# Optimization experiments

Measured on AMD Instinct MI355X. Metric: run time of the kernel, lower is better.

Reference implementation:

```python
import jax, jax.numpy as jnp
import numpy as np

INPUT_DIM = 2048
EMBED_DIM = 128


def setup_inputs() -> dict:
    key = jax.random.key(0)
    kx, kw, kb, kv = jax.random.split(key, 4)
    x = jax.random.normal(kx, (16384, INPUT_DIM), dtype=jnp.float32)
    # nn.Linear(input_dim, 1): weight [1, D] (init std=0.01), bias [1]
    W = jax.random.normal(kw, (1, INPUT_DIM), dtype=jnp.float32) * 0.01
    b = jax.random.normal(kb, (1,), dtype=jnp.float32) * 0.01
    # nn.Embedding(input_dim, embedding_dim): V [D, K] (init std=0.01)
    V = jax.random.normal(kv, (INPUT_DIM, EMBED_DIM), dtype=jnp.float32) * 0.01
    return {"x": x, "W": W, "b": b, "V": V}


def reference(x, W, b, V):
    # linear part: x @ W^T + b -> [B, 1]
    linear_part = x @ W.T + b
    # FM 2nd-order interaction via the standard identity:
    # 0.5 * sum_k ( (sum_d x_d V_dk)^2 - sum_d x_d^2 V_dk^2 )
    # equals the original sum_square - square_sum over weighted embeddings.
    xv = x @ V                       # [B, K]
    x2v2 = (x * x) @ (V * V)         # [B, K]
    interaction = 0.5 * jnp.sum(xv * xv - x2v2, axis=1, keepdims=True)
    return linear_part + interaction
```

## Files before the change

### kernel.cpp

```cpp
#include <hip/hip_runtime.h>
#include <hip/hip_bf16.h>

#define K_DIM 2048
#define N_DIM 128
#define BM 32
#define BK 64
#define NTILES (K_DIM / BK)
#define VT_CHUNK 16384

typedef __bf16 bf16x8 __attribute__((ext_vector_type(8)));
typedef float f32x4 __attribute__((ext_vector_type(4)));

__device__ __forceinline__ float dot4(f32x4 a, f32x4 b) {
    return a.x * b.x + a.y * b.y + a.z * b.z + a.w * b.w;
}

__device__ __forceinline__ void gload16(const void* g, void* lds) {
    __builtin_amdgcn_global_load_lds(
        (const __attribute__((address_space(1))) unsigned int*)g,
        (__attribute__((address_space(3))) unsigned int*)lds,
        16, 0, 0);
}

__global__ __launch_bounds__(256) void fm_prep(const float* __restrict__ V,
                                               char* __restrict__ VtS,
                                               float* __restrict__ s) {
    __shared__ float tile[64][132];
    const int t = threadIdx.x;
    const int kb = blockIdx.x;
    const int k0 = kb * 64;
#pragma unroll
    for (int i = 0; i < 8; ++i) {
        int idx = i * 256 + t;
        int kk = idx >> 5;
        int nq = (idx & 31) * 4;
        *(f32x4*)&tile[kk][nq] = *(const f32x4*)(V + (size_t)(k0 + kk) * N_DIM + nq);
    }
    __syncthreads();
    {
        const int n = t >> 1;
        const int half = t & 1;
        const int sw = (n & 7) << 4;
        char* dstbase = VtS + (size_t)kb * VT_CHUNK + n * 128;
#pragma unroll
        for (int g = 0; g < 4; ++g) {
            int kkg = half * 32 + g * 8;
            bf16x8 o;
#pragma unroll
            for (int e = 0; e < 8; ++e) o[e] = (__bf16)tile[kkg + e][n];
            *(bf16x8*)(dstbase + ((kkg * 2) ^ sw)) = o;
        }
    }
    if (t < 64) {
        float a = 0.f;
#pragma unroll
        for (int nq = 0; nq < 32; ++nq) {
            f32x4 v = *(f32x4*)&tile[t][nq * 4];
            a += dot4(v, v);
        }
        s[k0 + t] = a;
    }
}

__global__ __launch_bounds__(512, 4) void fm_main(const float* __restrict__ x,
                                                  const float* __restrict__ W,
                                                  const float* __restrict__ bptr,
                                                  const char* __restrict__ VtS,
                                                  const float* __restrict__ s,
                                                  float* __restrict__ out) {
    __shared__ __align__(16) char xbuf[2][8192];
    __shared__ __align__(16) char vbuf[2][16384];
    __shared__ __align__(16) float Wl[2048];
    __shared__ __align__(16) float Sl[2048];
    __shared__ float lin_lds[2][16];
    __shared__ float sq_lds[2][16];
    __shared__ float ss_lds[2][4][16];

    const int tid = threadIdx.x;
    const int w = tid >> 6;
    const int l = tid & 63;
    const int lr = l & 15;
    const int lg = l >> 4;
    const int wr = w >> 2;
    const int wc = w & 3;
    const int row0 = blockIdx.x * BM;

    *(f32x4*)&Wl[tid * 4] = *(const f32x4*)(W + tid * 4);
    *(f32x4*)&Sl[tid * 4] = *(const f32x4*)(s + tid * 4);

    const bool isX = (w < 4);
    const char* src[4];
    int loff[4];
    if (isX) {
#pragma unroll
        for (int j = 0; j < 2; ++j) {
            int gi = w * 2 + j;
            int rowt = gi * 4 + lg;
            int koff = (lr * 16) ^ ((rowt & 7) << 4);
            src[j] = (const char*)x + (size_t)(row0 + rowt) * (K_DIM * 4) + koff;
            loff[j] = gi * 1024;
        }
    } else {
#pragma unroll
        for (int j = 0; j < 4; ++j) {
            int vi = (w - 4) * 4 + j;
            src[j] = VtS + vi * 1024 + l * 16;
            loff[j] = vi * 1024;
        }
    }

    f32x4 acc[2];
    acc[0] = (f32x4){0.f, 0.f, 0.f, 0.f};
    acc[1] = (f32x4){0.f, 0.f, 0.f, 0.f};
    float lin = 0.f, sq = 0.f;

    if (isX) {
#pragma unroll
        for (int j = 0; j < 2; ++j) gload16(src[j], &xbuf[0][loff[j]]);
    } else {
#pragma unroll
        for (int j = 0; j < 4; ++j) gload16(src[j], &vbuf[0][loff[j]]);
    }
    __syncthreads();

    const int rowt = wr * 16 + lr;
    const int swA = (rowt & 7) << 4;

    for (int t = 0; t < NTILES; ++t) {
        const int cur = t & 1;
        if (t < NTILES - 1) {
            if (isX) {
#pragma unroll
                for (int j = 0; j < 2; ++j)
                    gload16(src[j] + (size_t)(t + 1) * (BK * 4), &xbuf[cur ^ 1][loff[j]]);
            } else {
#pragma unroll
                for (int j = 0; j < 4; ++j)
                    gload16(src[j] + (size_t)(t + 1) * VT_CHUNK, &vbuf[cur ^ 1][loff[j]]);
            }
        }

        const char* arow = &xbuf[cur][0] + rowt * 256;
        const char* vb = &vbuf[cur][0];

        bf16x8 af[2];
        f32x4 alo[2], ahi[2];
#pragma unroll
        for (int kb = 0; kb < 2; ++kb) {
            const int kA = kb * 128 + lg * 32;
            alo[kb] = *(const f32x4*)(arow + (kA ^ swA));
            ahi[kb] = *(const f32x4*)(arow + ((kA + 16) ^ swA));
            af[kb][0] = (__bf16)alo[kb].x; af[kb][1] = (__bf16)alo[kb].y;
            af[kb][2] = (__bf16)alo[kb].z; af[kb][3] = (__bf16)alo[kb].w;
            af[kb][4] = (__bf16)ahi[kb].x; af[kb][5] = (__bf16)ahi[kb].y;
            af[kb][6] = (__bf16)ahi[kb].z; af[kb][7] = (__bf16)ahi[kb].w;
        }
        if (wc == 0) {
            const int ki = t * 64 + lg * 8;
#pragma unroll
            for (int kb = 0; kb < 2; ++kb) {
                f32x4 w0 = *(const f32x4*)&Wl[ki + kb * 32];
                f32x4 w1 = *(const f32x4*)&Wl[ki + kb * 32 + 4];
                f32x4 s0 = *(const f32x4*)&Sl[ki + kb * 32];
                f32x4 s1 = *(const f32x4*)&Sl[ki + kb * 32 + 4];
                lin += dot4(alo[kb], w0) + dot4(ahi[kb], w1);
                sq  += dot4(alo[kb] * alo[kb], s0) + dot4(ahi[kb] * ahi[kb], s1);
            }
        }
#pragma unroll
        for (int c = 0; c < 2; ++c) {
            const int nt = wc * 32 + c * 16 + lr;
            const int swB = (nt & 7) << 4;
            const char* brow = vb + nt * 128;
#pragma unroll
            for (int kb = 0; kb < 2; ++kb) {
                bf16x8 bf = *(const bf16x8*)(brow + ((kb * 64 + lg * 16) ^ swB));
                acc[c] = __builtin_amdgcn_mfma_f32_16x16x32_bf16(af[kb], bf, acc[c], 0, 0, 0);
            }
        }
        __syncthreads();
    }

    f32x4 vss = acc[0] * acc[0] + acc[1] * acc[1];
#pragma unroll
    for (int m = 1; m < 16; m <<= 1) {
        vss.x += __shfl_xor(vss.x, m);
        vss.y += __shfl_xor(vss.y, m);
        vss.z += __shfl_xor(vss.z, m);
        vss.w += __shfl_xor(vss.w, m);
    }
    if (lr == 0) {
        ss_lds[wr][wc][lg * 4 + 0] = vss.x;
        ss_lds[wr][wc][lg * 4 + 1] = vss.y;
        ss_lds[wr][wc][lg * 4 + 2] = vss.z;
        ss_lds[wr][wc][lg * 4 + 3] = vss.w;
    }
    if (wc == 0) {
        lin += __shfl_xor(lin, 16); lin += __shfl_xor(lin, 32);
        sq  += __shfl_xor(sq, 16);  sq  += __shfl_xor(sq, 32);
        if (l < 16) { lin_lds[wr][l] = lin; sq_lds[wr][l] = sq; }
    }
    __syncthreads();
    if (tid < BM) {
        const int wrI = tid >> 4, r16 = tid & 15;
        out[row0 + tid] = lin_lds[wrI][r16] + bptr[0]
            + 0.5f * (ss_lds[wrI][0][r16] + ss_lds[wrI][1][r16]
                      + ss_lds[wrI][2][r16] + ss_lds[wrI][3][r16]
                      - sq_lds[wrI][r16]);
    }
}

extern "C" void kernel_launch(void* const* d_in, const int* in_sizes, int n_in,
                              void* d_out, int out_size, void* d_ws, size_t ws_size,
                              hipStream_t stream) {
    const float* x = (const float*)d_in[0];
    const float* W = (const float*)d_in[1];
    const float* b = (const float*)d_in[2];
    const float* V = (const float*)d_in[3];
    float* out = (float*)d_out;

    char* VtS = (char*)d_ws;
    float* s = (float*)((char*)d_ws + 32 * VT_CHUNK);

    fm_prep<<<32, 256, 0, stream>>>(V, VtS, s);
    fm_main<<<512, 512, 0, stream>>>(x, W, b, VtS, s, out);
}
```

Measured before the change: 204.8 us.

## Triple-buffer x tiles with prefetch distance two and explicit vmcnt waits

The x tile loads into LDS move from double to triple buffering, so x is prefetched two tiles ahead while V stays double-buffered. The __syncthreads at the end of each iteration becomes an explicit s_waitcnt vmcnt on only the older loads, followed by s_barrier, so newer loads can stay in flight across the barrier. The goal is to hide global memory latency on the streaming x input, which dominates traffic. This costs 8 KB more LDS per block, which may limit occupancy at 4 blocks per CU, and the hand-written waitcnt counts must match the number of outstanding loads exactly.

```diff
diff --git a/kernel.cpp b/kernel.cpp
--- a/kernel.cpp
+++ b/kernel.cpp
@@ -68,7 +68,7 @@
                                                   const char* __restrict__ VtS,
                                                   const float* __restrict__ s,
                                                   float* __restrict__ out) {
-    __shared__ __align__(16) char xbuf[2][8192];
+    __shared__ __align__(16) char xbuf[3][8192];
     __shared__ __align__(16) char vbuf[2][16384];
     __shared__ __align__(16) float Wl[2048];
     __shared__ __align__(16) float Sl[2048];
@@ -117,31 +117,38 @@
     if (isX) {
 #pragma unroll
         for (int j = 0; j < 2; ++j) gload16(src[j], &xbuf[0][loff[j]]);
+#pragma unroll
+        for (int j = 0; j < 2; ++j) gload16(src[j] + 256, &xbuf[1][loff[j]]);
+        asm volatile("s_waitcnt vmcnt(2) lgkmcnt(0)" ::: "memory");
     } else {
 #pragma unroll
         for (int j = 0; j < 4; ++j) gload16(src[j], &vbuf[0][loff[j]]);
-    }
-    __syncthreads();
+        asm volatile("s_waitcnt vmcnt(0) lgkmcnt(0)" ::: "memory");
+    }
+    __builtin_amdgcn_s_barrier();
+    __builtin_amdgcn_sched_barrier(0);
 
     const int rowt = wr * 16 + lr;
     const int swA = (rowt & 7) << 4;
 
+    int xr = 0, xi = 2, vr = 0;
     for (int t = 0; t < NTILES; ++t) {
-        const int cur = t & 1;
-        if (t < NTILES - 1) {
-            if (isX) {
+        if (isX) {
+            if (t + 2 < NTILES) {
 #pragma unroll
                 for (int j = 0; j < 2; ++j)
-                    gload16(src[j] + (size_t)(t + 1) * (BK * 4), &xbuf[cur ^ 1][loff[j]]);
-            } else {
+                    gload16(src[j] + (size_t)(t + 2) * (BK * 4), &xbuf[xi][loff[j]]);
+            }
+        } else {
+            if (t + 1 < NTILES) {
 #pragma unroll
                 for (int j = 0; j < 4; ++j)
-                    gload16(src[j] + (size_t)(t + 1) * VT_CHUNK, &vbuf[cur ^ 1][loff[j]]);
-            }
-        }
-
-        const char* arow = &xbuf[cur][0] + rowt * 256;
-        const char* vb = &vbuf[cur][0];
+                    gload16(src[j] + (size_t)(t + 1) * VT_CHUNK, &vbuf[vr ^ 1][loff[j]]);
+            }
+        }
+
+        const char* arow = &xbuf[xr][0] + rowt * 256;
+        const char* vb = &vbuf[vr][0];
 
         bf16x8 af[2];
         f32x4 alo[2], ahi[2];
@@ -178,7 +185,22 @@
                 acc[c] = __builtin_amdgcn_mfma_f32_16x16x32_bf16(af[kb], bf, acc[c], 0, 0, 0);
             }
         }
-        __syncthreads();
+
+        if (t < NTILES - 1) {
+            if (isX) {
+                if (t + 2 < NTILES)
+                    asm volatile("s_waitcnt vmcnt(2)" ::: "memory");
+                else
+                    asm volatile("s_waitcnt vmcnt(0)" ::: "memory");
+            } else {
+                asm volatile("s_waitcnt vmcnt(0)" ::: "memory");
+            }
+            __builtin_amdgcn_s_barrier();
+            __builtin_amdgcn_sched_barrier(0);
+        }
+        xr = (xr == 2) ? 0 : xr + 1;
+        xi = (xi == 2) ? 0 : xi + 1;
+        vr ^= 1;
     }
 
     f32x4 vss = acc[0] * acc[0] + acc[1] * acc[1];
```

New measurement: 206.5 us. No clear change (+0.8%).
